# Performance work log

Hardware: AMD Instinct MI355X
Metric: run time of the kernel (lower is better)

The kernel has to match this reference:

```python
import jax, jax.numpy as jnp
import numpy as np

B, N, D = 16, 8192, 64
M, S = 256, 32          # npoints, nsample
OUT = 128
RADIUS = 0.4
WC = 64                 # WeightNet output channels
BN_EPS = 1e-5
_BN_SCALE = 1.0 / np.sqrt(1.0 + BN_EPS)  # eval-mode BN, running mean 0 / var 1


def _bn(x, gamma, beta):
    shp = [1] * x.ndim
    shp[1] = -1
    return gamma.reshape(shp) * (x * _BN_SCALE) + beta.reshape(shp)


def _pdist2(a, b):
    # a (B,P,3), b (B,Q,3) -> (B,P,Q) squared distances
    return (jnp.sum(a * a, -1)[:, :, None] + jnp.sum(b * b, -1)[:, None, :]
            - 2.0 * jnp.einsum('bpd,bqd->bpq', a, b))


def _fps(xyz, npoints):
    # furthest point sampling, pointnet2 semantics (start at index 0)
    Bq, Nq, _ = xyz.shape
    first = jnp.zeros((Bq,), jnp.int32)

    def step(carry, _):
        dist, last = carry
        pt = xyz[jnp.arange(Bq), last]                   # (B,3)
        d = jnp.sum((xyz - pt[:, None, :]) ** 2, -1)
        dist = jnp.minimum(dist, d)
        nxt = jnp.argmax(dist, -1).astype(jnp.int32)
        return (dist, nxt), nxt

    init = (jnp.full((Bq, Nq), 1e10, xyz.dtype), first)
    _, rest = jax.lax.scan(step, init, None, length=npoints - 1)
    return jnp.concatenate([first[None], rest], 0).T     # (B, npoints)


def _ball_query(xyz, new_xyz, radius, nsample):
    # first `nsample` indices within radius, pad by repeating first valid index
    d2 = _pdist2(new_xyz, xyz)                           # (B,M,N)
    n = xyz.shape[1]
    key = jnp.where(d2 <= radius * radius, n - jnp.arange(n, dtype=jnp.int32), 0)
    vals, idx = jax.lax.top_k(key, nsample)              # lowest in-radius indices first
    return jnp.where(vals > 0, idx, idx[:, :, :1])


def _group(x_ch, idx):
    # x_ch (B,C,N), idx (B,M,S) -> (B,C,M,S)
    return jax.vmap(lambda f, i: f[:, i])(x_ch, idx)


def setup_inputs():
    key = jax.random.key(0)
    ks = jax.random.split(key, 8)
    f = jnp.float32

    def w(k, o, i):
        return (jax.random.normal(k, (o, i), f) / np.sqrt(i)).astype(f)

    return {
        'xyz': jax.random.uniform(ks[0], (B, N, 3), f),
        'feature': jax.random.normal(ks[1], (B, D, N), f),
        'w0': w(ks[2], WC, 3), 'b0': jnp.zeros((WC,), f), 'gamma0': jnp.ones((WC,), f), 'beta0': jnp.zeros((WC,), f),
        'w1': w(ks[3], WC, WC), 'b1': jnp.zeros((WC,), f), 'gamma1': jnp.ones((WC,), f), 'beta1': jnp.zeros((WC,), f),
        'w2': w(ks[4], WC, WC), 'b2': jnp.zeros((WC,), f),
        'wl': w(ks[5], OUT, D * WC), 'bl': jnp.zeros((OUT,), f), 'gammal': jnp.ones((OUT,), f), 'betal': jnp.zeros((OUT,), f),
        'wf': w(ks[6], OUT, D + OUT), 'bf': jnp.zeros((OUT,), f), 'gammaf': jnp.ones((OUT,), f), 'betaf': jnp.zeros((OUT,), f),
    }


def reference(xyz, feature, w0, b0, gamma0, beta0, w1, b1, gamma1, beta1, w2, b2,
              wl, bl, gammal, betal, wf, bf, gammaf, betaf):
    relu = jax.nn.relu
    # ---- furthest point sampling ----
    fidx = _fps(xyz, M)                                  # (B,M)
    new_xyz = xyz[jnp.arange(B)[:, None], fidx]          # (B,M,3)
    # ---- ball query + grouping ----
    gidx = _ball_query(xyz, new_xyz, RADIUS, S)          # (B,M,S)
    xyz_ch = jnp.transpose(xyz, (0, 2, 1))               # (B,3,N)
    grouped_xyz = _group(xyz_ch, gidx) - jnp.transpose(new_xyz, (0, 2, 1))[:, :, :, None]  # (B,3,M,S) centered
    grouped_feat = _group(feature, gidx)                 # (B,D,M,S)
    # ---- WeightNet (1x1 convs on offsets) ----
    h = relu(_bn(jnp.einsum('oc,bcms->boms', w0, grouped_xyz) + b0[None, :, None, None], gamma0, beta0))
    h = relu(_bn(jnp.einsum('oc,bcms->boms', w1, h) + b1[None, :, None, None], gamma1, beta1))
    weights = jnp.einsum('oc,bcms->boms', w2, h) + b2[None, :, None, None]  # (B,WC,M,S)
    # ---- weighted aggregation: (B,M,D,S) @ (B,M,S,WC) -> (B,M,D*WC) ----
    agg = jnp.einsum('bdms,bwms->bmdw', grouped_feat, weights).reshape(B, M, D * WC)
    new_feature = relu(_bn(jnp.einsum('od,bmd->bom', wl, agg) + bl[None, :, None], gammal, betal))  # (B,OUT,M)
    # ---- three-NN interpolation back to N points ----
    d2 = _pdist2(xyz, new_xyz)                           # (B,N,M)
    negd, nidx = jax.lax.top_k(-d2, 3)                   # 3 nearest sampled centers
    rd = 1.0 / (-negd + 1e-8)                            # reverse density on squared distance
    wts = rd / jnp.sum(rd, -1, keepdims=True)            # (B,N,3)
    gathered = jax.vmap(lambda f2, i: f2[:, i])(new_feature, nidx)  # (B,OUT,N,3)
    interp = jnp.einsum('bcnk,bnk->bcn', gathered, wts)  # (B,OUT,N)
    # ---- concat skip + final 1x1 conv ----
    cat = jnp.concatenate([interp, feature], 1)          # (B,OUT+D,N)
    return relu(_bn(jnp.einsum('oc,bcn->bon', wf, cat) + bf[None, :, None], gammaf, betaf))
```

## Files before the change

### kernel.cpp

```cpp
#include <hip/hip_runtime.h>
#include <hip/hip_bf16.h>
#include <cstdint>
#include <cstddef>

#define BB   16
#define NN   8192
#define DD   64
#define MM   256
#define SS   32
#define OUTC 128
#define WCC  64

using short8 = __attribute__((ext_vector_type(8))) short;
using f32x4  = __attribute__((ext_vector_type(4))) float;

#ifndef __has_builtin
#define __has_builtin(x) 0
#endif
#if __has_builtin(__builtin_amdgcn_update_dpp) && __has_builtin(__builtin_amdgcn_readlane)
#define USE_DPP 1
#else
#define USE_DPP 0
#endif

__device__ __forceinline__ float bnf(float x, float g, float be){
    const float BNS = 0.99999500003749969f;
    return g * (x * BNS) + be;
}
__device__ __forceinline__ unsigned short f2bf(float f){
    __hip_bfloat16 h = __float2bfloat16(f);
    return *reinterpret_cast<unsigned short*>(&h);
}
__device__ __forceinline__ float bf2f(unsigned short u){
    return __uint_as_float(((unsigned)u) << 16);
}

#define PRE_GRID (16 + 2048 + 512 + 24)

__global__ __launch_bounds__(256) void k_pre(const float* __restrict__ xyz, float* __restrict__ nxyz,
    const float* __restrict__ feature, unsigned short* __restrict__ featB,
    const float* __restrict__ wl, unsigned short* __restrict__ wlB,
    const float* __restrict__ wf, unsigned short* __restrict__ wfB){
  __shared__ union {
    struct {
      float sxyz[NN*3];
      float snew[MM*3];
      unsigned long long skey[2][4];
    } f;
    float tile[64][65];
  } sm;
  const int t = threadIdx.x;
  int blk = blockIdx.x;

  if (blk < 16){
    const int b = blk;
    const float* xb = xyz + (size_t)b*NN*3;
    for (int i = t; i < NN*3; i += 256) sm.f.sxyz[i] = xb[i];
    float px[32], py[32], pz[32], dist[32];
#pragma unroll
    for (int i=0;i<32;i++){
      int id = i*256 + t;
      px[i] = xb[id*3+0]; py[i] = xb[id*3+1]; pz[i] = xb[id*3+2];
      dist[i] = 1e10f;
    }
    __syncthreads();
    float lx = sm.f.sxyz[0], ly = sm.f.sxyz[1], lz = sm.f.sxyz[2];
    if (t==0){ sm.f.snew[0]=lx; sm.f.snew[1]=ly; sm.f.snew[2]=lz; }
    for (int step=1; step<MM; ++step){
      float bv = 0.0f; int bi = NN-1;
#pragma unroll
      for (int i=0;i<32;i++){
        float dx=px[i]-lx, dy=py[i]-ly, dz=pz[i]-lz;
        float d = dx*dx + dy*dy + dz*dz;
        float nd = fminf(dist[i], d);
        dist[i] = nd;
        bool gt = nd > bv;
        bv = gt ? nd : bv;
        bi = gt ? (i*256 + t) : bi;
      }
      unsigned long long key;
#if USE_DPP
      {
        float v = bv;
        int s_;
        s_ = __builtin_amdgcn_update_dpp(__float_as_int(v), __float_as_int(v), 0x111, 0xF, 0xF, 0); v = fmaxf(v, __int_as_float(s_));
        s_ = __builtin_amdgcn_update_dpp(__float_as_int(v), __float_as_int(v), 0x112, 0xF, 0xF, 0); v = fmaxf(v, __int_as_float(s_));
        s_ = __builtin_amdgcn_update_dpp(__float_as_int(v), __float_as_int(v), 0x114, 0xF, 0xF, 0); v = fmaxf(v, __int_as_float(s_));
        s_ = __builtin_amdgcn_update_dpp(__float_as_int(v), __float_as_int(v), 0x118, 0xF, 0xF, 0); v = fmaxf(v, __int_as_float(s_));
        s_ = __builtin_amdgcn_update_dpp(__float_as_int(v), __float_as_int(v), 0x142, 0xF, 0xF, 0); v = fmaxf(v, __int_as_float(s_));
        s_ = __builtin_amdgcn_update_dpp(__float_as_int(v), __float_as_int(v), 0x143, 0xF, 0xF, 0); v = fmaxf(v, __int_as_float(s_));
        float wmax = __int_as_float(__builtin_amdgcn_readlane(__float_as_int(v), 63));
        unsigned cm = (bv == wmax) ? (unsigned)bi : 0xFFFFFFFFu;
        unsigned u_;
        u_ = (unsigned)__builtin_amdgcn_update_dpp((int)cm, (int)cm, 0x111, 0xF, 0xF, 0); cm = cm < u_ ? cm : u_;
        u_ = (unsigned)__builtin_amdgcn_update_dpp((int)cm, (int)cm, 0x112, 0xF, 0xF, 0); cm = cm < u_ ? cm : u_;
        u_ = (unsigned)__builtin_amdgcn_update_dpp((int)cm, (int)cm, 0x114, 0xF, 0xF, 0); cm = cm < u_ ? cm : u_;
        u_ = (unsigned)__builtin_amdgcn_update_dpp((int)cm, (int)cm, 0x118, 0xF, 0xF, 0); cm = cm < u_ ? cm : u_;
        u_ = (unsigned)__builtin_amdgcn_update_dpp((int)cm, (int)cm, 0x142, 0xF, 0xF, 0); cm = cm < u_ ? cm : u_;
        u_ = (unsigned)__builtin_amdgcn_update_dpp((int)cm, (int)cm, 0x143, 0xF, 0xF, 0); cm = cm < u_ ? cm : u_;
        unsigned widx = (unsigned)__builtin_amdgcn_readlane((int)cm, 63);
        key = ((unsigned long long)__float_as_uint(wmax) << 32) | (unsigned)(NN-1 - widx);
      }
#else
      key = ((unsigned long long)__float_as_uint(bv) << 32) | (unsigned)(NN-1 - bi);
#pragma unroll
      for (int off=1; off<64; off<<=1){
        unsigned long long ok = __shfl_xor(key, off, 64);
        if (ok > key) key = ok;
      }
#endif
      const int p = step & 1;
      if ((t & 63) == 0) sm.f.skey[p][t>>6] = key;
      __syncthreads();
      unsigned long long k0=sm.f.skey[p][0], k1=sm.f.skey[p][1], k2=sm.f.skey[p][2], k3=sm.f.skey[p][3];
      unsigned long long ka = k0>k1?k0:k1, kb = k2>k3?k2:k3;
      unsigned long long kw = ka>kb?ka:kb;
      const int bid = (NN-1) - (int)(unsigned)(kw & 0xFFFFFFFFull);
      lx = sm.f.sxyz[bid*3+0]; ly = sm.f.sxyz[bid*3+1]; lz = sm.f.sxyz[bid*3+2];
      if (t==0){ sm.f.snew[step*3+0]=lx; sm.f.snew[step*3+1]=ly; sm.f.snew[step*3+2]=lz; }
    }
    __syncthreads();
    for (int i = t; i < MM*3; i += 256) nxyz[(size_t)b*MM*3 + i] = sm.f.snew[i];
    return;
  }
  blk -= 16;
  if (blk < 2048){
    const int b  = blk >> 7;
    const int n0 = (blk & 127) << 6;
    {
      const int d = t >> 2, j0 = (t & 3) << 4;
      const float* src = feature + ((size_t)b*DD + d)*NN + n0 + j0;
#pragma unroll
      for (int i=0;i<16;i+=4){
        float4 v = *(const float4*)(src + i);
        sm.tile[d][j0+i+0]=v.x; sm.tile[d][j0+i+1]=v.y; sm.tile[d][j0+i+2]=v.z; sm.tile[d][j0+i+3]=v.w;
      }
    }
    __syncthreads();
    {
      const int j = t >> 2, d0 = (t & 3) << 4;
      unsigned short hv[16];
#pragma unroll
      for (int i=0;i<16;i++) hv[i] = f2bf(sm.tile[d0+i][j]);
      unsigned short* dst = featB + ((size_t)b*NN + n0 + j)*64 + d0;
      *(uint4*)(dst)     = *(uint4*)(&hv[0]);
      *(uint4*)(dst + 8) = *(uint4*)(&hv[8]);
    }
    return;
  }
  blk -= 2048;
  if (blk < 512){
    int idx = (blk*256 + t)*4;
    float4 v = *(const float4*)(wl + idx);
    ushort4 h = make_ushort4(f2bf(v.x), f2bf(v.y), f2bf(v.z), f2bf(v.w));
    *(ushort4*)(wlB + idx) = h;
    return;
  }
  blk -= 512;
  {
    int idx = (blk*256 + t)*4;
    if (idx < 128*192){
      float4 v = *(const float4*)(wf + idx);
      ushort4 h = make_ushort4(f2bf(v.x), f2bf(v.y), f2bf(v.z), f2bf(v.w));
      *(ushort4*)(wfB + idx) = h;
    }
  }
}

__global__ __launch_bounds__(64) void k_bq_mlp(const float* __restrict__ xyz,
    const float* __restrict__ nxyz,
    const float* __restrict__ w0, const float* __restrict__ b0,
    const float* __restrict__ g0, const float* __restrict__ be0,
    const float* __restrict__ w1, const float* __restrict__ b1,
    const float* __restrict__ g1, const float* __restrict__ be1,
    const float* __restrict__ w2, const float* __restrict__ b2,
    int* __restrict__ gidx, float* __restrict__ wbuf){
  const int bm = blockIdx.x;
  const int b  = bm >> 8;
  const int c  = threadIdx.x;
  __shared__ int   sidx[SS];
  __shared__ float sgx[3][SS];
  __shared__ float sh0[SS][WCC];
  __shared__ float sh1[SS][WCC];

  const float w0r0 = w0[c*3+0], w0r1 = w0[c*3+1], w0r2 = w0[c*3+2];
  const float b0c=b0[c], g0c=g0[c], be0c=be0[c];
  const float b1c=b1[c], g1c=g1[c], be1c=be1[c], b2c=b2[c];
  float w1r[64], w2r[64];
#pragma unroll
  for (int i=0;i<16;i++){
    float4 v = *(const float4*)(w1 + c*64 + i*4);
    w1r[i*4+0]=v.x; w1r[i*4+1]=v.y; w1r[i*4+2]=v.z; w1r[i*4+3]=v.w;
    float4 u = *(const float4*)(w2 + c*64 + i*4);
    w2r[i*4+0]=u.x; w2r[i*4+1]=u.y; w2r[i*4+2]=u.z; w2r[i*4+3]=u.w;
  }
  const float cx = nxyz[bm*3+0], cy = nxyz[bm*3+1], cz = nxyz[bm*3+2];
  const float* xb = xyz + (size_t)b*NN*3;
  const float R2 = (float)(0.4*0.4);
  int cnt = 0;
  for (int n0=0; n0<NN && cnt<SS; n0+=64){
    int n = n0 + c;
    float dx = xb[n*3+0]-cx, dy = xb[n*3+1]-cy, dz = xb[n*3+2]-cz;
    float d2 = dx*dx+dy*dy+dz*dz;
    bool in = (d2 <= R2);
    unsigned long long mk = __ballot(in);
    int rank = cnt + (int)__popcll(mk & ((1ull<<c)-1ull));
    if (in && rank < SS) sidx[rank] = n;
    cnt += (int)__popcll(mk);
  }
  int total = min(cnt, SS);
  __syncthreads();
  int i0 = sidx[0];
  if (c >= total && c < SS) sidx[c] = i0;
  __syncthreads();
  if (c < SS){
    int p = sidx[c];
    gidx[bm*SS + c] = p;
    sgx[0][c] = xb[p*3+0]-cx;
    sgx[1][c] = xb[p*3+1]-cy;
    sgx[2][c] = xb[p*3+2]-cz;
  }
  __syncthreads();
  for (int s=0;s<SS;s++){
    float pre = w0r0*sgx[0][s] + w0r1*sgx[1][s] + w0r2*sgx[2][s] + b0c;
    sh0[s][c] = fmaxf(bnf(pre, g0c, be0c), 0.f);
  }
  __syncthreads();
  for (int s=0;s<SS;s++){
    float a = b1c;
#pragma unroll
    for (int k=0;k<64;k+=4){
      float4 h = *(const float4*)(&sh0[s][k]);
      a += w1r[k]*h.x + w1r[k+1]*h.y + w1r[k+2]*h.z + w1r[k+3]*h.w;
    }
    sh1[s][c] = fmaxf(bnf(a, g1c, be1c), 0.f);
  }
  __syncthreads();
  float* wb = wbuf + (size_t)bm*SS*WCC;
  for (int s=0;s<SS;s++){
    float a = b2c;
#pragma unroll
    for (int k=0;k<64;k+=4){
      float4 h = *(const float4*)(&sh1[s][k]);
      a += w2r[k]*h.x + w2r[k+1]*h.y + w2r[k+2]*h.z + w2r[k+3]*h.w;
    }
    wb[s*WCC + c] = a;
  }
}

__global__ __launch_bounds__(256) void k_agg(const unsigned short* __restrict__ featB,
                                             const float* __restrict__ wbuf,
                                             const int* __restrict__ gidx,
                                             unsigned short* __restrict__ aggB){
  const int bm = blockIdx.x;
  const int b  = bm >> 8;
  __shared__ float wt[SS][WCC];
  __shared__ int   sidx[SS];
  const int t = threadIdx.x;
  const float* wsrc = wbuf + (size_t)bm*SS*WCC;
#pragma unroll
  for (int i=0;i<8;i++){
    int li = t + i*256;
    ((float*)wt)[li] = wsrc[li];
  }
  if (t < SS) sidx[t] = gidx[bm*SS + t];
  __syncthreads();
  const int d  = t & 63;
  const int wg = t >> 6;
  float acc[16];
#pragma unroll
  for (int j=0;j<16;j++) acc[j]=0.f;
  const unsigned short* fb = featB + (size_t)b*NN*64;
  for (int s=0;s<SS;s++){
    float fv = bf2f(fb[(size_t)sidx[s]*64 + d]);
#pragma unroll
    for (int j=0;j<16;j++) acc[j] += fv * wt[s][wg*16+j];
  }
  unsigned short h[16];
#pragma unroll
  for (int j=0;j<16;j++) h[j] = f2bf(acc[j]);
  unsigned short* ab = aggB + (size_t)bm*4096 + d*64 + wg*16;
  *(uint4*)(ab)     = *(uint4*)(&h[0]);
  *(uint4*)(ab + 8) = *(uint4*)(&h[8]);
}

__global__ __launch_bounds__(256) void k_nf_part(const unsigned short* __restrict__ aggB,
                                                 const unsigned short* __restrict__ wlB,
                                                 float* __restrict__ part){
  const int blk = blockIdx.x;
  const int rb  = blk >> 2;
  const int ks  = blk & 3;
  const int wid = threadIdx.x >> 6, lane = threadIdx.x & 63;
  const int m0 = rb*64 + wid*16;
  const int r  = lane & 15, kg = lane >> 4;
  f32x4 acc[8];
#pragma unroll
  for (int i=0;i<8;i++) acc[i] = (f32x4){0.f,0.f,0.f,0.f};
  const short* arow = (const short*)aggB + (size_t)(m0 + r)*4096 + ks*1024 + kg*8;
  const short* brow = (const short*)wlB  + (size_t)r*4096        + ks*1024 + kg*8;
#pragma unroll 4
  for (int kc=0; kc<32; kc++){
    short8 a = *(const short8*)(arow + kc*32);
#pragma unroll
    for (int ot=0; ot<8; ot++){
      short8 bfr = *(const short8*)(brow + (size_t)ot*16*4096 + kc*32);
      acc[ot] = __builtin_amdgcn_mfma_f32_16x16x32_bf16(a, bfr, acc[ot], 0, 0, 0);
    }
  }
  float* pb = part + ((size_t)ks << 19);
#pragma unroll
  for (int ot=0; ot<8; ot++){
#pragma unroll
    for (int rr=0; rr<4; rr++){
      int row = m0 + kg*4 + rr;
      pb[(size_t)row*128 + ot*16 + r] = acc[ot][rr];
    }
  }
}

__global__ __launch_bounds__(256) void k_nf_ep(const float* __restrict__ part,
    const float* __restrict__ bl, const float* __restrict__ gl, const float* __restrict__ bel,
    float* __restrict__ nfT){
  const int gid = blockIdx.x*256 + threadIdx.x;
  const int base = gid*4;
  const int o0 = base & 127;
  float4 s0 = *(const float4*)(part + base);
  float4 s1 = *(const float4*)(part + (1<<19) + base);
  float4 s2 = *(const float4*)(part + (2<<19) + base);
  float4 s3 = *(const float4*)(part + (3<<19) + base);
  float sum[4] = {s0.x+s1.x+s2.x+s3.x, s0.y+s1.y+s2.y+s3.y,
                  s0.z+s1.z+s2.z+s3.z, s0.w+s1.w+s2.w+s3.w};
  float ov[4];
#pragma unroll
  for (int j=0;j<4;j++){
    const int o = o0 + j;
    ov[j] = fmaxf(bnf(sum[j] + bl[o], gl[o], bel[o]), 0.f);
  }
  *(float4*)(nfT + base) = make_float4(ov[0],ov[1],ov[2],ov[3]);
}

__global__ __launch_bounds__(256) void k_final(const float* __restrict__ xyz,
    const float* __restrict__ nxyz, const float* __restrict__ nfT,
    const unsigned short* __restrict__ featB, const unsigned short* __restrict__ wfB,
    const float* __restrict__ bf, const float* __restrict__ gf, const float* __restrict__ bef,
    float* __restrict__ out){
  const int blk = blockIdx.x;
  const int b  = blk >> 6;
  const int n0 = (blk & 63) << 7;
  __shared__ float snew[MM*3];
  __shared__ float sw[128][3];
  __shared__ int   si[128][3];
  const int t = threadIdx.x;
  if (t < 192){
    float4 v = *(const float4*)(nxyz + (size_t)b*MM*3 + t*4);
    snew[t*4+0]=v.x; snew[t*4+1]=v.y; snew[t*4+2]=v.z; snew[t*4+3]=v.w;
  }
  __syncthreads();
  if (t < 128){
    const int n = n0 + t;
    const float x = xyz[((size_t)b*NN+n)*3+0];
    const float y = xyz[((size_t)b*NN+n)*3+1];
    const float z = xyz[((size_t)b*NN+n)*3+2];
    float d1=1e30f, d2=1e30f, d3=1e30f; int i1=0,i2=0,i3=0;
    for (int m=0;m<MM;m++){
      float dx=x-snew[m*3+0], dy=y-snew[m*3+1], dz=z-snew[m*3+2];
      float d = dx*dx+dy*dy+dz*dz;
      if (d < d3){
        if (d < d1){ d3=d2;i3=i2; d2=d1;i2=i1; d1=d;i1=m; }
        else if (d < d2){ d3=d2;i3=i2; d2=d;i2=m; }
        else { d3=d;i3=m; }
      }
    }
    float r1=1.f/(d1+1e-8f), r2=1.f/(d2+1e-8f), r3=1.f/(d3+1e-8f);
    float rs = 1.f/(r1+r2+r3);
    sw[t][0]=r1*rs; sw[t][1]=r2*rs; sw[t][2]=r3*rs;
    si[t][0]=i1; si[t][1]=i2; si[t][2]=i3;
  }
  __syncthreads();

  const int w = t >> 6, lane = t & 63;
  const int r = lane & 15, kg = lane >> 4;
  float wA[8][3]; int iA[8][3];
#pragma unroll
  for (int nt=0;nt<8;nt++){
    int n = nt*16 + r;
    wA[nt][0]=sw[n][0]; wA[nt][1]=sw[n][1]; wA[nt][2]=sw[n][2];
    iA[nt][0]=si[n][0]*128; iA[nt][1]=si[n][1]*128; iA[nt][2]=si[n][2]*128;
  }
  const float* nfb = nfT + (size_t)b*MM*128;
  const unsigned short* fbB = featB + ((size_t)b*NN + n0)*64;
  const unsigned short* wfRow0 = wfB + (size_t)(w*32 +      r)*192 + kg*8;
  const unsigned short* wfRow1 = wfB + (size_t)(w*32 + 16 + r)*192 + kg*8;
  f32x4 acc[2][8];
#pragma unroll
  for (int i=0;i<2;i++)
#pragma unroll
    for (int j=0;j<8;j++) acc[i][j] = (f32x4){0.f,0.f,0.f,0.f};

#pragma unroll
  for (int c=0;c<6;c++){
    short8 a0 = *(const short8*)(wfRow0 + c*32);
    short8 a1 = *(const short8*)(wfRow1 + c*32);
    if (c < 4){
      const int k8 = c*32 + kg*8;
#pragma unroll
      for (int nt=0;nt<8;nt++){
        const float* p0 = nfb + iA[nt][0] + k8;
        const float* p1 = nfb + iA[nt][1] + k8;
        const float* p2 = nfb + iA[nt][2] + k8;
        float4 xa = *(const float4*)(p0), xb4 = *(const float4*)(p0+4);
        float4 ya = *(const float4*)(p1), yb4 = *(const float4*)(p1+4);
        float4 za = *(const float4*)(p2), zb4 = *(const float4*)(p2+4);
        const float w0v=wA[nt][0], w1v=wA[nt][1], w2v=wA[nt][2];
        float e0 = w0v*xa.x + w1v*ya.x + w2v*za.x;
        float e1 = w0v*xa.y + w1v*ya.y + w2v*za.y;
        float e2 = w0v*xa.z + w1v*ya.z + w2v*za.z;
        float e3 = w0v*xa.w + w1v*ya.w + w2v*za.w;
        float e4 = w0v*xb4.x + w1v*yb4.x + w2v*zb4.x;
        float e5 = w0v*xb4.y + w1v*yb4.y + w2v*zb4.y;
        float e6 = w0v*xb4.z + w1v*yb4.z + w2v*zb4.z;
        float e7 = w0v*xb4.w + w1v*yb4.w + w2v*zb4.w;
        short8 bfr = { (short)f2bf(e0), (short)f2bf(e1), (short)f2bf(e2), (short)f2bf(e3),
                       (short)f2bf(e4), (short)f2bf(e5), (short)f2bf(e6), (short)f2bf(e7) };
        acc[0][nt] = __builtin_amdgcn_mfma_f32_16x16x32_bf16(a0, bfr, acc[0][nt], 0, 0, 0);
        acc[1][nt] = __builtin_amdgcn_mfma_f32_16x16x32_bf16(a1, bfr, acc[1][nt], 0, 0, 0);
      }
    } else {
      const int d8 = (c-4)*32 + kg*8;
#pragma unroll
      for (int nt=0;nt<8;nt++){
        short8 bfr = *(const short8*)(fbB + (size_t)(nt*16 + r)*64 + d8);
        acc[0][nt] = __builtin_amdgcn_mfma_f32_16x16x32_bf16(a0, bfr, acc[0][nt], 0, 0, 0);
        acc[1][nt] = __builtin_amdgcn_mfma_f32_16x16x32_bf16(a1, bfr, acc[1][nt], 0, 0, 0);
      }
    }
  }
#pragma unroll
  for (int ot=0; ot<2; ot++){
#pragma unroll
    for (int rr=0; rr<4; rr++){
      const int o = w*32 + ot*16 + kg*4 + rr;
      const float bfo = bf[o], gfo = gf[o], befo = bef[o];
      float* dst = out + ((size_t)b*OUTC + o)*NN + n0 + r;
#pragma unroll
      for (int nt=0;nt<8;nt++){
        float val = fmaxf(bnf(acc[ot][nt][rr] + bfo, gfo, befo), 0.f);
        dst[nt*16] = val;
      }
    }
  }
}

extern "C" void kernel_launch(void* const* d_in, const int* in_sizes, int n_in,
                              void* d_out, int out_size, void* d_ws, size_t ws_size,
                              hipStream_t stream){
  const float* xyz     = (const float*)d_in[0];
  const float* feature = (const float*)d_in[1];
  const float* w0  = (const float*)d_in[2];
  const float* b0  = (const float*)d_in[3];
  const float* g0  = (const float*)d_in[4];
  const float* be0 = (const float*)d_in[5];
  const float* w1  = (const float*)d_in[6];
  const float* b1  = (const float*)d_in[7];
  const float* g1  = (const float*)d_in[8];
  const float* be1 = (const float*)d_in[9];
  const float* w2  = (const float*)d_in[10];
  const float* b2  = (const float*)d_in[11];
  const float* wl  = (const float*)d_in[12];
  const float* bl  = (const float*)d_in[13];
  const float* gl  = (const float*)d_in[14];
  const float* bel = (const float*)d_in[15];
  const float* wf  = (const float*)d_in[16];
  const float* bf  = (const float*)d_in[17];
  const float* gf  = (const float*)d_in[18];
  const float* bef = (const float*)d_in[19];
  float* out = (float*)d_out;

  char* ws = (char*)d_ws;
  unsigned short* featB = (unsigned short*)(ws + 0);
  float*          wbuf  = (float*)(ws + 16777216);
  float*          part  = (float*)(ws + 16777216);
  unsigned short* aggB  = (unsigned short*)(ws + 50331648);
  unsigned short* wlB   = (unsigned short*)(ws + 83886080);
  unsigned short* wfB   = (unsigned short*)(ws + 84934656);
  float*          nxyz  = (float*)(ws + 84983808);
  int*            gidx  = (int*)  (ws + 85032960);
  float*          nfT   = (float*)(ws + 85557248);

  k_pre    <<<PRE_GRID, 256, 0, stream>>>(xyz, nxyz, feature, featB, wl, wlB, wf, wfB);
  k_bq_mlp <<<BB*MM, 64, 0, stream>>>(xyz, nxyz, w0,b0,g0,be0, w1,b1,g1,be1, w2,b2, gidx, wbuf);
  k_agg    <<<BB*MM, 256, 0, stream>>>(featB, wbuf, gidx, aggB);
  k_nf_part<<<256,  256, 0, stream>>>(aggB, wlB, part);
  k_nf_ep  <<<512,  256, 0, stream>>>(part, bl, gl, bel, nfT);
  k_final  <<<BB*(NN/128), 256, 0, stream>>>(xyz, nxyz, nfT, featB, wfB, bf, gf, bef, out);
}
```

Before: 592.6 us.

## Fuse ball-query MLP with aggregation and widen FPS block to 512 threads

Merges the ball-query/WeightNet kernel and the aggregation kernel into one 256-thread kernel. The weights stay in shared memory, so the wbuf and gidx global round trips and one launch go away, and the MLP work is spread across four wavefronts instead of one. The FPS pre-kernel moves to 512 threads with 16 points per thread and an 8-wave key reduction. This shortens the serial per-step loop at the cost of a wider cross-wave reduction and more barrier participants. The DPP fallback path is dropped, and the ball query still runs on one wave while the other three wait at the barrier.

```diff
diff --git a/kernel.cpp b/kernel.cpp
--- a/kernel.cpp
+++ b/kernel.cpp
@@ -14,15 +14,6 @@
 using short8 = __attribute__((ext_vector_type(8))) short;
 using f32x4  = __attribute__((ext_vector_type(4))) float;
 
-#ifndef __has_builtin
-#define __has_builtin(x) 0
-#endif
-#if __has_builtin(__builtin_amdgcn_update_dpp) && __has_builtin(__builtin_amdgcn_readlane)
-#define USE_DPP 1
-#else
-#define USE_DPP 0
-#endif
-
 __device__ __forceinline__ float bnf(float x, float g, float be){
     const float BNS = 0.99999500003749969f;
     return g * (x * BNS) + be;
@@ -35,9 +26,9 @@
     return __uint_as_float(((unsigned)u) << 16);
 }
 
-#define PRE_GRID (16 + 2048 + 512 + 24)
-
-__global__ __launch_bounds__(256) void k_pre(const float* __restrict__ xyz, float* __restrict__ nxyz,
+#define PRE_GRID (16 + 2048 + 256 + 12)
+
+__global__ __launch_bounds__(512) void k_pre(const float* __restrict__ xyz, float* __restrict__ nxyz,
     const float* __restrict__ feature, unsigned short* __restrict__ featB,
     const float* __restrict__ wl, unsigned short* __restrict__ wlB,
     const float* __restrict__ wf, unsigned short* __restrict__ wfB){
@@ -45,7 +36,7 @@
     struct {
       float sxyz[NN*3];
       float snew[MM*3];
-      unsigned long long skey[2][4];
+      unsigned long long skey[2][8];
     } f;
     float tile[64][65];
   } sm;
@@ -55,11 +46,11 @@
   if (blk < 16){
     const int b = blk;
     const float* xb = xyz + (size_t)b*NN*3;
-    for (int i = t; i < NN*3; i += 256) sm.f.sxyz[i] = xb[i];
-    float px[32], py[32], pz[32], dist[32];
-#pragma unroll
-    for (int i=0;i<32;i++){
-      int id = i*256 + t;
+    for (int i = t; i < NN*3; i += 512) sm.f.sxyz[i] = xb[i];
+    float px[16], py[16], pz[16], dist[16];
+#pragma unroll
+    for (int i=0;i<16;i++){
+      int id = i*512 + t;
       px[i] = xb[id*3+0]; py[i] = xb[id*3+1]; pz[i] = xb[id*3+2];
       dist[i] = 1e10f;
     }
@@ -69,58 +60,49 @@
     for (int step=1; step<MM; ++step){
       float bv = 0.0f; int bi = NN-1;
 #pragma unroll
-      for (int i=0;i<32;i++){
+      for (int i=0;i<16;i++){
         float dx=px[i]-lx, dy=py[i]-ly, dz=pz[i]-lz;
         float d = dx*dx + dy*dy + dz*dz;
         float nd = fminf(dist[i], d);
         dist[i] = nd;
         bool gt = nd > bv;
         bv = gt ? nd : bv;
-        bi = gt ? (i*256 + t) : bi;
-      }
-      unsigned long long key;
-#if USE_DPP
-      {
-        float v = bv;
-        int s_;
-        s_ = __builtin_amdgcn_update_dpp(__float_as_int(v), __float_as_int(v), 0x111, 0xF, 0xF, 0); v = fmaxf(v, __int_as_float(s_));
-        s_ = __builtin_amdgcn_update_dpp(__float_as_int(v), __float_as_int(v), 0x112, 0xF, 0xF, 0); v = fmaxf(v, __int_as_float(s_));
-        s_ = __builtin_amdgcn_update_dpp(__float_as_int(v), __float_as_int(v), 0x114, 0xF, 0xF, 0); v = fmaxf(v, __int_as_float(s_));
-        s_ = __builtin_amdgcn_update_dpp(__float_as_int(v), __float_as_int(v), 0x118, 0xF, 0xF, 0); v = fmaxf(v, __int_as_float(s_));
-        s_ = __builtin_amdgcn_update_dpp(__float_as_int(v), __float_as_int(v), 0x142, 0xF, 0xF, 0); v = fmaxf(v, __int_as_float(s_));
-        s_ = __builtin_amdgcn_update_dpp(__float_as_int(v), __float_as_int(v), 0x143, 0xF, 0xF, 0); v = fmaxf(v, __int_as_float(s_));
-        float wmax = __int_as_float(__builtin_amdgcn_readlane(__float_as_int(v), 63));
-        unsigned cm = (bv == wmax) ? (unsigned)bi : 0xFFFFFFFFu;
-        unsigned u_;
-        u_ = (unsigned)__builtin_amdgcn_update_dpp((int)cm, (int)cm, 0x111, 0xF, 0xF, 0); cm = cm < u_ ? cm : u_;
-        u_ = (unsigned)__builtin_amdgcn_update_dpp((int)cm, (int)cm, 0x112, 0xF, 0xF, 0); cm = cm < u_ ? cm : u_;
-        u_ = (unsigned)__builtin_amdgcn_update_dpp((int)cm, (int)cm, 0x114, 0xF, 0xF, 0); cm = cm < u_ ? cm : u_;
-        u_ = (unsigned)__builtin_amdgcn_update_dpp((int)cm, (int)cm, 0x118, 0xF, 0xF, 0); cm = cm < u_ ? cm : u_;
-        u_ = (unsigned)__builtin_amdgcn_update_dpp((int)cm, (int)cm, 0x142, 0xF, 0xF, 0); cm = cm < u_ ? cm : u_;
-        u_ = (unsigned)__builtin_amdgcn_update_dpp((int)cm, (int)cm, 0x143, 0xF, 0xF, 0); cm = cm < u_ ? cm : u_;
-        unsigned widx = (unsigned)__builtin_amdgcn_readlane((int)cm, 63);
-        key = ((unsigned long long)__float_as_uint(wmax) << 32) | (unsigned)(NN-1 - widx);
-      }
-#else
-      key = ((unsigned long long)__float_as_uint(bv) << 32) | (unsigned)(NN-1 - bi);
-#pragma unroll
-      for (int off=1; off<64; off<<=1){
-        unsigned long long ok = __shfl_xor(key, off, 64);
-        if (ok > key) key = ok;
-      }
-#endif
+        bi = gt ? (i*512 + t) : bi;
+      }
+      float v = bv; int s_;
+      s_ = __builtin_amdgcn_update_dpp(__float_as_int(v), __float_as_int(v), 0x111, 0xF, 0xF, 0); v = fmaxf(v, __int_as_float(s_));
+      s_ = __builtin_amdgcn_update_dpp(__float_as_int(v), __float_as_int(v), 0x112, 0xF, 0xF, 0); v = fmaxf(v, __int_as_float(s_));
+      s_ = __builtin_amdgcn_update_dpp(__float_as_int(v), __float_as_int(v), 0x114, 0xF, 0xF, 0); v = fmaxf(v, __int_as_float(s_));
+      s_ = __builtin_amdgcn_update_dpp(__float_as_int(v), __float_as_int(v), 0x118, 0xF, 0xF, 0); v = fmaxf(v, __int_as_float(s_));
+      s_ = __builtin_amdgcn_update_dpp(__float_as_int(v), __float_as_int(v), 0x142, 0xF, 0xF, 0); v = fmaxf(v, __int_as_float(s_));
+      s_ = __builtin_amdgcn_update_dpp(__float_as_int(v), __float_as_int(v), 0x143, 0xF, 0xF, 0); v = fmaxf(v, __int_as_float(s_));
+      float wmax = __int_as_float(__builtin_amdgcn_readlane(__float_as_int(v), 63));
+      unsigned cm = (bv == wmax) ? (unsigned)bi : 0xFFFFFFFFu;
+      unsigned u_;
+      u_ = (unsigned)__builtin_amdgcn_update_dpp((int)cm, (int)cm, 0x111, 0xF, 0xF, 0); cm = cm < u_ ? cm : u_;
+      u_ = (unsigned)__builtin_amdgcn_update_dpp((int)cm, (int)cm, 0x112, 0xF, 0xF, 0); cm = cm < u_ ? cm : u_;
+      u_ = (unsigned)__builtin_amdgcn_update_dpp((int)cm, (int)cm, 0x114, 0xF, 0xF, 0); cm = cm < u_ ? cm : u_;
+      u_ = (unsigned)__builtin_amdgcn_update_dpp((int)cm, (int)cm, 0x118, 0xF, 0xF, 0); cm = cm < u_ ? cm : u_;
+      u_ = (unsigned)__builtin_amdgcn_update_dpp((int)cm, (int)cm, 0x142, 0xF, 0xF, 0); cm = cm < u_ ? cm : u_;
+      u_ = (unsigned)__builtin_amdgcn_update_dpp((int)cm, (int)cm, 0x143, 0xF, 0xF, 0); cm = cm < u_ ? cm : u_;
+      unsigned widx = (unsigned)__builtin_amdgcn_readlane((int)cm, 63);
+      unsigned long long key = ((unsigned long long)__float_as_uint(wmax) << 32) | (unsigned)(NN-1 - widx);
+
       const int p = step & 1;
       if ((t & 63) == 0) sm.f.skey[p][t>>6] = key;
       __syncthreads();
       unsigned long long k0=sm.f.skey[p][0], k1=sm.f.skey[p][1], k2=sm.f.skey[p][2], k3=sm.f.skey[p][3];
+      unsigned long long k4=sm.f.skey[p][4], k5=sm.f.skey[p][5], k6=sm.f.skey[p][6], k7=sm.f.skey[p][7];
       unsigned long long ka = k0>k1?k0:k1, kb = k2>k3?k2:k3;
-      unsigned long long kw = ka>kb?ka:kb;
+      unsigned long long kc = k4>k5?k4:k5, kd = k6>k7?k6:k7;
+      unsigned long long ke = ka>kb?ka:kb, kf = kc>kd?kc:kd;
+      unsigned long long kw = ke>kf?ke:kf;
       const int bid = (NN-1) - (int)(unsigned)(kw & 0xFFFFFFFFull);
       lx = sm.f.sxyz[bid*3+0]; ly = sm.f.sxyz[bid*3+1]; lz = sm.f.sxyz[bid*3+2];
       if (t==0){ sm.f.snew[step*3+0]=lx; sm.f.snew[step*3+1]=ly; sm.f.snew[step*3+2]=lz; }
     }
     __syncthreads();
-    for (int i = t; i < MM*3; i += 256) nxyz[(size_t)b*MM*3 + i] = sm.f.snew[i];
+    for (int i = t; i < MM*3; i += 512) nxyz[(size_t)b*MM*3 + i] = sm.f.snew[i];
     return;
   }
   blk -= 16;
@@ -128,37 +110,36 @@
     const int b  = blk >> 7;
     const int n0 = (blk & 127) << 6;
     {
-      const int d = t >> 2, j0 = (t & 3) << 4;
+      const int d = t >> 3, j0 = (t & 7) << 3;
       const float* src = feature + ((size_t)b*DD + d)*NN + n0 + j0;
 #pragma unroll
-      for (int i=0;i<16;i+=4){
+      for (int i=0;i<8;i+=4){
         float4 v = *(const float4*)(src + i);
         sm.tile[d][j0+i+0]=v.x; sm.tile[d][j0+i+1]=v.y; sm.tile[d][j0+i+2]=v.z; sm.tile[d][j0+i+3]=v.w;
       }
     }
     __syncthreads();
     {
-      const int j = t >> 2, d0 = (t & 3) << 4;
-      unsigned short hv[16];
-#pragma unroll
-      for (int i=0;i<16;i++) hv[i] = f2bf(sm.tile[d0+i][j]);
+      const int j = t >> 3, d0 = (t & 7) << 3;
+      unsigned short hv[8];
+#pragma unroll
+      for (int i=0;i<8;i++) hv[i] = f2bf(sm.tile[d0+i][j]);
       unsigned short* dst = featB + ((size_t)b*NN + n0 + j)*64 + d0;
-      *(uint4*)(dst)     = *(uint4*)(&hv[0]);
-      *(uint4*)(dst + 8) = *(uint4*)(&hv[8]);
+      *(uint4*)(dst) = *(uint4*)(&hv[0]);
     }
     return;
   }
   blk -= 2048;
-  if (blk < 512){
-    int idx = (blk*256 + t)*4;
+  if (blk < 256){
+    int idx = (blk*512 + t)*4;
     float4 v = *(const float4*)(wl + idx);
     ushort4 h = make_ushort4(f2bf(v.x), f2bf(v.y), f2bf(v.z), f2bf(v.w));
     *(ushort4*)(wlB + idx) = h;
     return;
   }
-  blk -= 512;
+  blk -= 256;
   {
-    int idx = (blk*256 + t)*4;
+    int idx = (blk*512 + t)*4;
     if (idx < 128*192){
       float4 v = *(const float4*)(wf + idx);
       ushort4 h = make_ushort4(f2bf(v.x), f2bf(v.y), f2bf(v.z), f2bf(v.w));
@@ -167,21 +148,25 @@
   }
 }
 
-__global__ __launch_bounds__(64) void k_bq_mlp(const float* __restrict__ xyz,
+__global__ __launch_bounds__(256) void k_group(const float* __restrict__ xyz,
     const float* __restrict__ nxyz,
     const float* __restrict__ w0, const float* __restrict__ b0,
     const float* __restrict__ g0, const float* __restrict__ be0,
     const float* __restrict__ w1, const float* __restrict__ b1,
     const float* __restrict__ g1, const float* __restrict__ be1,
     const float* __restrict__ w2, const float* __restrict__ b2,
-    int* __restrict__ gidx, float* __restrict__ wbuf){
+    const unsigned short* __restrict__ featB,
+    unsigned short* __restrict__ aggB){
   const int bm = blockIdx.x;
   const int b  = bm >> 8;
-  const int c  = threadIdx.x;
+  const int t  = threadIdx.x;
+  const int c  = t & 63;
+  const int wg = t >> 6;
   __shared__ int   sidx[SS];
   __shared__ float sgx[3][SS];
   __shared__ float sh0[SS][WCC];
   __shared__ float sh1[SS][WCC];
+  __shared__ float swt[SS][WCC];
 
   const float w0r0 = w0[c*3+0], w0r1 = w0[c*3+1], w0r2 = w0[c*3+2];
   const float b0c=b0[c], g0c=g0[c], be0c=be0[c];
@@ -194,39 +179,43 @@
     float4 u = *(const float4*)(w2 + c*64 + i*4);
     w2r[i*4+0]=u.x; w2r[i*4+1]=u.y; w2r[i*4+2]=u.z; w2r[i*4+3]=u.w;
   }
-  const float cx = nxyz[bm*3+0], cy = nxyz[bm*3+1], cz = nxyz[bm*3+2];
-  const float* xb = xyz + (size_t)b*NN*3;
-  const float R2 = (float)(0.4*0.4);
-  int cnt = 0;
-  for (int n0=0; n0<NN && cnt<SS; n0+=64){
-    int n = n0 + c;
-    float dx = xb[n*3+0]-cx, dy = xb[n*3+1]-cy, dz = xb[n*3+2]-cz;
-    float d2 = dx*dx+dy*dy+dz*dz;
-    bool in = (d2 <= R2);
-    unsigned long long mk = __ballot(in);
-    int rank = cnt + (int)__popcll(mk & ((1ull<<c)-1ull));
-    if (in && rank < SS) sidx[rank] = n;
-    cnt += (int)__popcll(mk);
-  }
-  int total = min(cnt, SS);
-  __syncthreads();
-  int i0 = sidx[0];
-  if (c >= total && c < SS) sidx[c] = i0;
-  __syncthreads();
-  if (c < SS){
-    int p = sidx[c];
-    gidx[bm*SS + c] = p;
-    sgx[0][c] = xb[p*3+0]-cx;
-    sgx[1][c] = xb[p*3+1]-cy;
-    sgx[2][c] = xb[p*3+2]-cz;
-  }
-  __syncthreads();
-  for (int s=0;s<SS;s++){
+
+  if (t < 64){
+    const float cx = nxyz[bm*3+0], cy = nxyz[bm*3+1], cz = nxyz[bm*3+2];
+    const float* xb = xyz + (size_t)b*NN*3;
+    const float R2 = (float)(0.4*0.4);
+    int cnt = 0;
+    for (int n0=0; n0<NN && cnt<SS; n0+=64){
+      int n = n0 + c;
+      float dx = xb[n*3+0]-cx, dy = xb[n*3+1]-cy, dz = xb[n*3+2]-cz;
+      float d2 = dx*dx+dy*dy+dz*dz;
+      bool in = (d2 <= R2);
+      unsigned long long mk = __ballot(in);
+      int rank = cnt + (int)__popcll(mk & ((1ull<<c)-1ull));
+      if (in && rank < SS) sidx[rank] = n;
+      cnt += (int)__popcll(mk);
+    }
+    int total = min(cnt, SS);
+    int i0 = sidx[0];
+    if (c >= total && c < SS) sidx[c] = i0;
+    if (c < SS){
+      int p = sidx[c];
+      sgx[0][c] = xb[p*3+0]-cx;
+      sgx[1][c] = xb[p*3+1]-cy;
+      sgx[2][c] = xb[p*3+2]-cz;
+    }
+  }
+  __syncthreads();
+#pragma unroll
+  for (int i=0;i<8;i++){
+    const int s = i*4 + wg;
     float pre = w0r0*sgx[0][s] + w0r1*sgx[1][s] + w0r2*sgx[2][s] + b0c;
     sh0[s][c] = fmaxf(bnf(pre, g0c, be0c), 0.f);
   }
   __syncthreads();
-  for (int s=0;s<SS;s++){
+#pragma unroll
+  for (int i=0;i<8;i++){
+    const int s = i*4 + wg;
     float a = b1c;
 #pragma unroll
     for (int k=0;k<64;k+=4){
@@ -236,37 +225,19 @@
     sh1[s][c] = fmaxf(bnf(a, g1c, be1c), 0.f);
   }
   __syncthreads();
-  float* wb = wbuf + (size_t)bm*SS*WCC;
-  for (int s=0;s<SS;s++){
+#pragma unroll
+  for (int i=0;i<8;i++){
+    const int s = i*4 + wg;
     float a = b2c;
 #pragma unroll
     for (int k=0;k<64;k+=4){
       float4 h = *(const float4*)(&sh1[s][k]);
       a += w2r[k]*h.x + w2r[k+1]*h.y + w2r[k+2]*h.z + w2r[k+3]*h.w;
     }
-    wb[s*WCC + c] = a;
-  }
-}
-
-__global__ __launch_bounds__(256) void k_agg(const unsigned short* __restrict__ featB,
-                                             const float* __restrict__ wbuf,
-                                             const int* __restrict__ gidx,
-                                             unsigned short* __restrict__ aggB){
-  const int bm = blockIdx.x;
-  const int b  = bm >> 8;
-  __shared__ float wt[SS][WCC];
-  __shared__ int   sidx[SS];
-  const int t = threadIdx.x;
-  const float* wsrc = wbuf + (size_t)bm*SS*WCC;
-#pragma unroll
-  for (int i=0;i<8;i++){
-    int li = t + i*256;
-    ((float*)wt)[li] = wsrc[li];
-  }
-  if (t < SS) sidx[t] = gidx[bm*SS + t];
-  __syncthreads();
-  const int d  = t & 63;
-  const int wg = t >> 6;
+    swt[s][c] = a;
+  }
+  __syncthreads();
+  const int d = c;
   float acc[16];
 #pragma unroll
   for (int j=0;j<16;j++) acc[j]=0.f;
@@ -274,7 +245,7 @@
   for (int s=0;s<SS;s++){
     float fv = bf2f(fb[(size_t)sidx[s]*64 + d]);
 #pragma unroll
-    for (int j=0;j<16;j++) acc[j] += fv * wt[s][wg*16+j];
+    for (int j=0;j<16;j++) acc[j] += fv * swt[s][wg*16+j];
   }
   unsigned short h[16];
 #pragma unroll
@@ -478,18 +449,15 @@
 
   char* ws = (char*)d_ws;
   unsigned short* featB = (unsigned short*)(ws + 0);
-  float*          wbuf  = (float*)(ws + 16777216);
-  float*          part  = (float*)(ws + 16777216);
-  unsigned short* aggB  = (unsigned short*)(ws + 50331648);
-  unsigned short* wlB   = (unsigned short*)(ws + 83886080);
-  unsigned short* wfB   = (unsigned short*)(ws + 84934656);
-  float*          nxyz  = (float*)(ws + 84983808);
-  int*            gidx  = (int*)  (ws + 85032960);
-  float*          nfT   = (float*)(ws + 85557248);
-
-  k_pre    <<<PRE_GRID, 256, 0, stream>>>(xyz, nxyz, feature, featB, wl, wlB, wf, wfB);
-  k_bq_mlp <<<BB*MM, 64, 0, stream>>>(xyz, nxyz, w0,b0,g0,be0, w1,b1,g1,be1, w2,b2, gidx, wbuf);
-  k_agg    <<<BB*MM, 256, 0, stream>>>(featB, wbuf, gidx, aggB);
+  unsigned short* aggB  = (unsigned short*)(ws + 16777216);
+  float*          part  = (float*)(ws + 50331648);
+  unsigned short* wlB   = (unsigned short*)(ws + 58720256);
+  unsigned short* wfB   = (unsigned short*)(ws + 59768832);
+  float*          nxyz  = (float*)(ws + 59817984);
+  float*          nfT   = (float*)(ws + 59867136);
+
+  k_pre    <<<PRE_GRID, 512, 0, stream>>>(xyz, nxyz, feature, featB, wl, wlB, wf, wfB);
+  k_group  <<<BB*MM, 256, 0, stream>>>(xyz, nxyz, w0,b0,g0,be0, w1,b1,g1,be1, w2,b2, featB, aggB);
   k_nf_part<<<256,  256, 0, stream>>>(aggB, wlB, part);
   k_nf_ep  <<<512,  256, 0, stream>>>(part, bl, gl, bel, nfT);
   k_final  <<<BB*(NN/128), 256, 0, stream>>>(xyz, nxyz, nfT, featB, wfB, bf, gf, bef, out);
```

Result: slower. 621.3 us (+4.8%).
